# Kernel tuning notes

Hardware: AMD Instinct MI355X
Metric: run time of the kernel (lower is better)

Reference implementation:

```python
import jax, jax.numpy as jnp
import numpy as np

INPUT_DIM, CB_DIM, CB_VOCAB = 512, 16, 8192
N = 16384
EPS = 1e-12  # F.normalize default eps


def setup_inputs() -> dict:
    key = jax.random.key(0)
    kx, kp, kc = jax.random.split(key, 3)
    x = jax.random.normal(kx, (N, INPUT_DIM), dtype=jnp.float32)
    # xavier_uniform_ on P [input_dim, cb_dim]
    bound = float(np.sqrt(6.0 / (INPUT_DIM + CB_DIM)))
    P = jax.random.uniform(kp, (INPUT_DIM, CB_DIM), dtype=jnp.float32,
                           minval=-bound, maxval=bound)
    # CB = F.normalize(randn(cb_vocab, cb_dim)) -> unit rows
    CB = jax.random.normal(kc, (CB_VOCAB, CB_DIM), dtype=jnp.float32)
    CB = CB / jnp.maximum(jnp.linalg.norm(CB, axis=1, keepdims=True), EPS)
    return {"x": x, "P": P, "CB": CB}


def reference(x, P, CB):
    # random projection: [N, input_dim] @ [input_dim, cb_dim] -> [N, cb_dim]
    xp = x @ P
    # L2-normalize projected vectors (rows)
    xp = xp / jnp.maximum(jnp.linalg.norm(xp, axis=1, keepdims=True), EPS)
    # cosine similarity against unit-norm codebook = plain dot product
    sim = xp @ CB.T  # [N, cb_vocab]
    return jnp.argmax(sim, axis=1)  # [N] int codebook indices
```

## Files before the change

kernel.cpp:

```cpp
#include <hip/hip_runtime.h>
#include <stdint.h>

#define N_ROWS   16384
#define IN_DIM   512
#define CB_DIM   16
#define CB_VOCAB 8192

#define PREP_BLOCKS 128
#define PROJ_BLOCKS 256

#define N_RT   (N_ROWS / 16)
#define N_CT   (CB_VOCAB / 16)
#define CODEPARTS 32
#define CT_PER_PART (N_CT / CODEPARTS)
#define N_ROWGRP 64

#define WS_OFF_AFA  0
#define WS_OFF_AFB  (1u << 20)
#define WS_OFF_BHH  (2u << 20)
#define WS_OFF_B31  ((2u << 20) + (512u << 10))
#define WS_OFF_PART (3u << 20)
#define WS_OFF_CNT  ((3u << 20) + (128u << 10))
#define WS_OFF_PF   ((3u << 20) + (192u << 10))

typedef __attribute__((ext_vector_type(8))) short bf16x8;
typedef __attribute__((ext_vector_type(4))) float f32x4;

__device__ __forceinline__ unsigned fkey(float f) {
    unsigned u = __float_as_uint(f);
    return (u & 0x80000000u) ? ~u : (u | 0x80000000u);
}

__device__ __forceinline__ unsigned short f2bf(float f) {
    unsigned u = __float_as_uint(f);
    return (unsigned short)((u + 0x7FFFu + ((u >> 16) & 1u)) >> 16);
}
__device__ __forceinline__ float bf2f(unsigned short h) {
    return __uint_as_float(((unsigned)h) << 16);
}

__global__ __launch_bounds__(256, 2)
void k_prep(const float* __restrict__ P, const float* __restrict__ CB,
            bf16x8* __restrict__ Bhh, bf16x8* __restrict__ B31,
            bf16x8* __restrict__ Pf,
            unsigned long long* __restrict__ part, unsigned* __restrict__ cnt) {
    const int pb   = blockIdx.x;
    const int wave = threadIdx.x >> 6;
    const int lane = threadIdx.x & 63;

    if (threadIdx.x < 128) part[pb * 128 + threadIdx.x] = 0ull;
    if (pb == 0 && threadIdx.x < 64) cnt[threadIdx.x] = 0u;

    {
        const int ct   = pb * 4 + wave;
        const int n    = lane & 15;
        const int quad = lane >> 4;
        const int kh   = (quad & 1) * 8;
        const int lvl  = quad >> 1;
        const int code = ct * 16 + n;

        const float4* b4 = (const float4*)(CB + (size_t)code * CB_DIM + kh);
        float4 a = b4[0], b = b4[1];
        float v[8] = {a.x, a.y, a.z, a.w, b.x, b.y, b.z, b.w};

        bf16x8 shh, s31;
#pragma unroll
        for (int j = 0; j < 8; ++j) {
            float f = v[j];
            unsigned short b1 = f2bf(f);  float r1 = f - bf2f(b1);
            unsigned short b2 = f2bf(r1); float r2 = r1 - bf2f(b2);
            unsigned short b3 = f2bf(r2);
            shh[j] = (short)(lvl ? b2 : b1);
            s31[j] = (short)(lvl ? b1 : b3);
        }
        Bhh[(size_t)ct * 64 + lane] = shh;
        B31[(size_t)ct * 64 + lane] = s31;
    }

    const int gslot = pb * 256 + threadIdx.x;
    if (gslot < 1024) {
        const int c  = gslot >> 6;
        const int l  = gslot & 63;
        const int n  = l & 15;
        const int kq = l >> 4;
        const int k0 = c * 32 + kq * 8;

        bf16x8 p1, p2, p3;
#pragma unroll
        for (int j = 0; j < 8; ++j) {
            float f = P[(size_t)(k0 + j) * CB_DIM + n];
            unsigned short b1 = f2bf(f);  float r1 = f - bf2f(b1);
            unsigned short b2 = f2bf(r1); float r2 = r1 - bf2f(b2);
            unsigned short b3 = f2bf(r2);
            p1[j] = (short)b1; p2[j] = (short)b2; p3[j] = (short)b3;
        }
        Pf[gslot]        = p1;
        Pf[1024 + gslot] = p2;
        Pf[2048 + gslot] = p3;
    }
}

__global__ __launch_bounds__(256, 1)
void k_proj(const float* __restrict__ x, const bf16x8* __restrict__ Pf,
            bf16x8* __restrict__ AfragA, bf16x8* __restrict__ AfragB) {
    __shared__ float xpL[4][16][20];
    const int wave = threadIdx.x >> 6;
    const int lane = threadIdx.x & 63;
    const int rt   = blockIdx.x * 4 + wave;
    const int m    = lane & 15;
    const int kq   = lane >> 4;

    const float4* xr =
        (const float4*)(x + (size_t)(rt * 16 + m) * IN_DIM) + kq * 2;

    f32x4 acc1 = {0.f, 0.f, 0.f, 0.f};
    f32x4 acc2 = {0.f, 0.f, 0.f, 0.f};

    float4 xf0[4], xf1[4];
#pragma unroll
    for (int c = 0; c < 4; ++c) { xf0[c] = xr[c * 8]; xf1[c] = xr[c * 8 + 1]; }

#pragma unroll
    for (int c = 0; c < 16; ++c) {
        bf16x8 p1 = Pf[c * 64 + lane];
        bf16x8 p2 = Pf[1024 + c * 64 + lane];
        bf16x8 p3 = Pf[2048 + c * 64 + lane];

        float4 xa = xf0[c & 3], xb = xf1[c & 3];
        if (c + 4 < 16) {
            xf0[c & 3] = xr[(c + 4) * 8];
            xf1[c & 3] = xr[(c + 4) * 8 + 1];
        }

        float xs[8] = {xa.x, xa.y, xa.z, xa.w, xb.x, xb.y, xb.z, xb.w};
        bf16x8 a1, a2, a3;
#pragma unroll
        for (int j = 0; j < 8; ++j) {
            float f = xs[j];
            unsigned short b1 = f2bf(f);  float r1 = f - bf2f(b1);
            unsigned short b2 = f2bf(r1); float r2 = r1 - bf2f(b2);
            unsigned short b3 = f2bf(r2);
            a1[j] = (short)b1; a2[j] = (short)b2; a3[j] = (short)b3;
        }

        acc1 = __builtin_amdgcn_mfma_f32_16x16x32_bf16(a1, p1, acc1, 0, 0, 0);
        acc2 = __builtin_amdgcn_mfma_f32_16x16x32_bf16(a1, p2, acc2, 0, 0, 0);
        acc1 = __builtin_amdgcn_mfma_f32_16x16x32_bf16(a2, p1, acc1, 0, 0, 0);
        acc2 = __builtin_amdgcn_mfma_f32_16x16x32_bf16(a1, p3, acc2, 0, 0, 0);
        acc1 = __builtin_amdgcn_mfma_f32_16x16x32_bf16(a2, p2, acc1, 0, 0, 0);
        acc2 = __builtin_amdgcn_mfma_f32_16x16x32_bf16(a3, p1, acc2, 0, 0, 0);
    }

#pragma unroll
    for (int r = 0; r < 4; ++r)
        xpL[wave][kq * 4 + r][m] = acc1[r] + acc2[r];

    asm volatile("s_waitcnt lgkmcnt(0)" ::: "memory");
    __builtin_amdgcn_sched_barrier(0);

    const int kh  = (kq & 1) * 8;
    const int lvl = kq >> 1;
    bf16x8 sa, sb;
#pragma unroll
    for (int j = 0; j < 8; ++j) {
        float f = xpL[wave][m][kh + j];
        unsigned short b1 = f2bf(f);  float r1 = f - bf2f(b1);
        unsigned short b2 = f2bf(r1); float r2 = r1 - bf2f(b2);
        unsigned short b3 = f2bf(r2);
        sa[j] = (short)(lvl ? b2 : b1);
        sb[j] = (short)(lvl ? b3 : b1);
    }
    AfragA[(size_t)rt * 64 + lane] = sa;
    AfragB[(size_t)rt * 64 + lane] = sb;
}

__global__ __launch_bounds__(256, 4)
void k_scan(const bf16x8* __restrict__ AfragA, const bf16x8* __restrict__ AfragB,
            const bf16x8* __restrict__ Bhh, const bf16x8* __restrict__ B31,
            unsigned long long* __restrict__ part, unsigned* __restrict__ cnt,
            int* __restrict__ out) {
    __shared__ int s_done;
    const int codepart = blockIdx.x & (CODEPARTS - 1);
    const int rowgrp   = blockIdx.x >> 5;
    const int wave     = threadIdx.x >> 6;
    const int lane     = threadIdx.x & 63;
    const int n        = lane & 15;
    const int quad     = lane >> 4;
    const int rt_base  = rowgrp * 16 + wave * 4;

    bf16x8 Aa[4], Ab[4];
#pragma unroll
    for (int t = 0; t < 4; ++t) {
        Aa[t] = AfragA[(size_t)(rt_base + t) * 64 + lane];
        Ab[t] = AfragB[(size_t)(rt_base + t) * 64 + lane];
    }

    float bestv[4][4];
    int   bestc[4][4];
#pragma unroll
    for (int t = 0; t < 4; ++t)
#pragma unroll
        for (int r = 0; r < 4; ++r) { bestv[t][r] = -INFINITY; bestc[t][r] = 0; }

    const int ct0 = codepart * CT_PER_PART;
    size_t ib = (size_t)ct0 * 64;
    bf16x8 nb1  = Bhh[ib + lane];
    bf16x8 nb1s = Bhh[ib + (lane ^ 32)];
    bf16x8 nb3  = B31[ib + lane];

    for (int c = 0; c < CT_PER_PART; ++c) {
        bf16x8 b1 = nb1, b1s = nb1s, b3 = nb3;
        if (c + 1 < CT_PER_PART) {
            size_t ibn = (size_t)(ct0 + c + 1) * 64;
            nb1  = Bhh[ibn + lane];
            nb1s = Bhh[ibn + (lane ^ 32)];
            nb3  = B31[ibn + lane];
        }
#pragma unroll
        for (int t = 0; t < 4; ++t) {
            f32x4 s = __builtin_amdgcn_mfma_f32_16x16x32_bf16(
                          Aa[t], b1, (f32x4){0.f, 0.f, 0.f, 0.f}, 0, 0, 0);
            s = __builtin_amdgcn_mfma_f32_16x16x32_bf16(Aa[t], b1s, s, 0, 0, 0);
            s = __builtin_amdgcn_mfma_f32_16x16x32_bf16(Ab[t], b3,  s, 0, 0, 0);
#pragma unroll
            for (int r = 0; r < 4; ++r) {
                if (s[r] > bestv[t][r]) { bestv[t][r] = s[r]; bestc[t][r] = c; }
            }
        }
    }

#pragma unroll
    for (int t = 0; t < 4; ++t) {
#pragma unroll
        for (int r = 0; r < 4; ++r) {
            unsigned code = (unsigned)(codepart * (CT_PER_PART * 16) +
                                       bestc[t][r] * 16 + n);
            unsigned long long packed =
                ((unsigned long long)fkey(bestv[t][r]) << 32) |
                (unsigned long long)(0xFFFFFFFFu - code);
#pragma unroll
            for (int mk = 1; mk <= 8; mk <<= 1) {
                unsigned long long o = __shfl_xor(packed, mk, 64);
                packed = (o > packed) ? o : packed;
            }
            if (n == 0) {
                int row = (rt_base + t) * 16 + quad * 4 + r;
                atomicMax(&part[row], packed);
            }
        }
    }

    __syncthreads();
    if (threadIdx.x == 0)
        s_done = (atomicAdd(&cnt[rowgrp], 1u) == (unsigned)(CODEPARTS - 1));
    __syncthreads();

    if (s_done) {
        int row = rowgrp * 256 + threadIdx.x;
        unsigned long long v = atomicAdd(&part[row], 0ull);
        out[row] = (int)(0xFFFFFFFFu - (unsigned)(v & 0xFFFFFFFFull));
    }
}

extern "C" void kernel_launch(void* const* d_in, const int* in_sizes, int n_in,
                              void* d_out, int out_size, void* d_ws, size_t ws_size,
                              hipStream_t stream) {
    const float* x  = (const float*)d_in[0];
    const float* P  = (const float*)d_in[1];
    const float* CB = (const float*)d_in[2];
    int* out = (int*)d_out;

    char* ws = (char*)d_ws;
    bf16x8* AfragA = (bf16x8*)(ws + WS_OFF_AFA);
    bf16x8* AfragB = (bf16x8*)(ws + WS_OFF_AFB);
    bf16x8* Bhh    = (bf16x8*)(ws + WS_OFF_BHH);
    bf16x8* B31    = (bf16x8*)(ws + WS_OFF_B31);
    unsigned long long* part = (unsigned long long*)(ws + WS_OFF_PART);
    unsigned* cnt  = (unsigned*)(ws + WS_OFF_CNT);
    bf16x8* Pf     = (bf16x8*)(ws + WS_OFF_PF);

    k_prep<<<PREP_BLOCKS, 256, 0, stream>>>(P, CB, Bhh, B31, Pf, part, cnt);
    k_proj<<<PROJ_BLOCKS, 256, 0, stream>>>(x, Pf, AfragA, AfragB);
    k_scan<<<N_ROWGRP * CODEPARTS, 256, 0, stream>>>(
        AfragA, AfragB, Bhh, B31, part, cnt, out);
}
```

Before: 121.1 us.

## Fuse prep and projection kernels, split K across waves, deepen scan prefetch

Merges the codebook/P preprocessing kernel and the projection kernel into one launch. Each projection block now rebuilds the split-bf16 P fragments in shared memory and splits the K dimension across four waves, then reduces them through LDS. Codebook-conversion blocks run alongside as extra blocks. The scan kernel's codebook prefetch becomes two tiles deep and the loop is fully unrolled. This removes one launch and the inter-kernel dependency, and raises parallelism in the projection. In exchange, every one of the 1024 projection blocks redundantly converts P, and register pressure in the scan loop goes up.

```diff
diff --git a/kernel.cpp b/kernel.cpp
--- a/kernel.cpp
+++ b/kernel.cpp
@@ -6,10 +6,9 @@
 #define CB_DIM   16
 #define CB_VOCAB 8192
 
+#define PROJ_BLOCKS 1024
 #define PREP_BLOCKS 128
-#define PROJ_BLOCKS 256
-
-#define N_RT   (N_ROWS / 16)
+
 #define N_CT   (CB_VOCAB / 16)
 #define CODEPARTS 32
 #define CT_PER_PART (N_CT / CODEPARTS)
@@ -21,7 +20,6 @@
 #define WS_OFF_B31  ((2u << 20) + (512u << 10))
 #define WS_OFF_PART (3u << 20)
 #define WS_OFF_CNT  ((3u << 20) + (128u << 10))
-#define WS_OFF_PF   ((3u << 20) + (192u << 10))
 
 typedef __attribute__((ext_vector_type(8))) short bf16x8;
 typedef __attribute__((ext_vector_type(4))) float f32x4;
@@ -39,19 +37,24 @@
     return __uint_as_float(((unsigned)h) << 16);
 }
 
-__global__ __launch_bounds__(256, 2)
-void k_prep(const float* __restrict__ P, const float* __restrict__ CB,
-            bf16x8* __restrict__ Bhh, bf16x8* __restrict__ B31,
-            bf16x8* __restrict__ Pf,
-            unsigned long long* __restrict__ part, unsigned* __restrict__ cnt) {
-    const int pb   = blockIdx.x;
-    const int wave = threadIdx.x >> 6;
-    const int lane = threadIdx.x & 63;
-
-    if (threadIdx.x < 128) part[pb * 128 + threadIdx.x] = 0ull;
-    if (pb == 0 && threadIdx.x < 64) cnt[threadIdx.x] = 0u;
-
-    {
+__global__ __launch_bounds__(256, 3)
+void k_front(const float* __restrict__ x, const float* __restrict__ P,
+             const float* __restrict__ CB,
+             bf16x8* __restrict__ AfragA, bf16x8* __restrict__ AfragB,
+             bf16x8* __restrict__ Bhh, bf16x8* __restrict__ B31,
+             unsigned long long* __restrict__ part, unsigned* __restrict__ cnt) {
+    __shared__ bf16x8 sPf[3][1024];
+    __shared__ __align__(16) float foldb[1024];
+
+    const int tid  = threadIdx.x;
+    const int wave = tid >> 6;
+    const int lane = tid & 63;
+
+    if (blockIdx.x >= PROJ_BLOCKS) {
+        const int pb = blockIdx.x - PROJ_BLOCKS;
+        if (tid < 128) part[pb * 128 + tid] = 0ull;
+        if (pb == 0 && tid < 64) cnt[tid] = 0u;
+
         const int ct   = pb * 4 + wave;
         const int n    = lane & 15;
         const int quad = lane >> 4;
@@ -75,12 +78,14 @@
         }
         Bhh[(size_t)ct * 64 + lane] = shh;
         B31[(size_t)ct * 64 + lane] = s31;
-    }
-
-    const int gslot = pb * 256 + threadIdx.x;
-    if (gslot < 1024) {
-        const int c  = gslot >> 6;
-        const int l  = gslot & 63;
+        return;
+    }
+
+#pragma unroll
+    for (int s4 = 0; s4 < 4; ++s4) {
+        const int s  = tid + s4 * 256;
+        const int c  = s >> 6;
+        const int l  = s & 63;
         const int n  = l & 15;
         const int kq = l >> 4;
         const int k0 = c * 32 + kq * 8;
@@ -94,44 +99,33 @@
             unsigned short b3 = f2bf(r2);
             p1[j] = (short)b1; p2[j] = (short)b2; p3[j] = (short)b3;
         }
-        Pf[gslot]        = p1;
-        Pf[1024 + gslot] = p2;
-        Pf[2048 + gslot] = p3;
-    }
-}
-
-__global__ __launch_bounds__(256, 1)
-void k_proj(const float* __restrict__ x, const bf16x8* __restrict__ Pf,
-            bf16x8* __restrict__ AfragA, bf16x8* __restrict__ AfragB) {
-    __shared__ float xpL[4][16][20];
-    const int wave = threadIdx.x >> 6;
-    const int lane = threadIdx.x & 63;
-    const int rt   = blockIdx.x * 4 + wave;
-    const int m    = lane & 15;
-    const int kq   = lane >> 4;
-
-    const float4* xr =
-        (const float4*)(x + (size_t)(rt * 16 + m) * IN_DIM) + kq * 2;
+        sPf[0][s] = p1; sPf[1][s] = p2; sPf[2][s] = p3;
+    }
+    __syncthreads();
+
+    const int rt = blockIdx.x;
+    const int m  = lane & 15;
+    const int kq = lane >> 4;
+    const float4* xr = (const float4*)(x + (size_t)(rt * 16 + m) * IN_DIM);
+
+    float4 xf[8];
+#pragma unroll
+    for (int i = 0; i < 4; ++i) {
+        xf[2 * i]     = xr[(wave * 4 + i) * 8 + kq * 2];
+        xf[2 * i + 1] = xr[(wave * 4 + i) * 8 + kq * 2 + 1];
+    }
 
     f32x4 acc1 = {0.f, 0.f, 0.f, 0.f};
     f32x4 acc2 = {0.f, 0.f, 0.f, 0.f};
 
-    float4 xf0[4], xf1[4];
-#pragma unroll
-    for (int c = 0; c < 4; ++c) { xf0[c] = xr[c * 8]; xf1[c] = xr[c * 8 + 1]; }
-
-#pragma unroll
-    for (int c = 0; c < 16; ++c) {
-        bf16x8 p1 = Pf[c * 64 + lane];
-        bf16x8 p2 = Pf[1024 + c * 64 + lane];
-        bf16x8 p3 = Pf[2048 + c * 64 + lane];
-
-        float4 xa = xf0[c & 3], xb = xf1[c & 3];
-        if (c + 4 < 16) {
-            xf0[c & 3] = xr[(c + 4) * 8];
-            xf1[c & 3] = xr[(c + 4) * 8 + 1];
-        }
-
+#pragma unroll
+    for (int i = 0; i < 4; ++i) {
+        const int c = wave * 4 + i;
+        bf16x8 p1 = sPf[0][c * 64 + lane];
+        bf16x8 p2 = sPf[1][c * 64 + lane];
+        bf16x8 p3 = sPf[2][c * 64 + lane];
+
+        float4 xa = xf[2 * i], xb = xf[2 * i + 1];
         float xs[8] = {xa.x, xa.y, xa.z, xa.w, xb.x, xb.y, xb.z, xb.w};
         bf16x8 a1, a2, a3;
 #pragma unroll
@@ -151,27 +145,41 @@
         acc2 = __builtin_amdgcn_mfma_f32_16x16x32_bf16(a3, p1, acc2, 0, 0, 0);
     }
 
-#pragma unroll
-    for (int r = 0; r < 4; ++r)
-        xpL[wave][kq * 4 + r][m] = acc1[r] + acc2[r];
-
-    asm volatile("s_waitcnt lgkmcnt(0)" ::: "memory");
-    __builtin_amdgcn_sched_barrier(0);
-
-    const int kh  = (kq & 1) * 8;
-    const int lvl = kq >> 1;
-    bf16x8 sa, sb;
-#pragma unroll
-    for (int j = 0; j < 8; ++j) {
-        float f = xpL[wave][m][kh + j];
-        unsigned short b1 = f2bf(f);  float r1 = f - bf2f(b1);
-        unsigned short b2 = f2bf(r1); float r2 = r1 - bf2f(b2);
-        unsigned short b3 = f2bf(r2);
-        sa[j] = (short)(lvl ? b2 : b1);
-        sb[j] = (short)(lvl ? b3 : b1);
-    }
-    AfragA[(size_t)rt * 64 + lane] = sa;
-    AfragB[(size_t)rt * 64 + lane] = sb;
+    *(f32x4*)&foldb[(wave * 64 + lane) * 4] = acc1 + acc2;
+    __syncthreads();
+
+    if (wave == 0) {
+        f32x4 s0 = *(const f32x4*)&foldb[(0 * 64 + lane) * 4];
+        f32x4 s1 = *(const f32x4*)&foldb[(1 * 64 + lane) * 4];
+        f32x4 s2 = *(const f32x4*)&foldb[(2 * 64 + lane) * 4];
+        f32x4 s3 = *(const f32x4*)&foldb[(3 * 64 + lane) * 4];
+        f32x4 sum = ((s0 + s1) + s2) + s3;
+
+        asm volatile("s_waitcnt lgkmcnt(0)" ::: "memory");
+        __builtin_amdgcn_sched_barrier(0);
+
+#pragma unroll
+        for (int r = 0; r < 4; ++r)
+            foldb[(kq * 4 + r) * 20 + m] = sum[r];
+
+        asm volatile("s_waitcnt lgkmcnt(0)" ::: "memory");
+        __builtin_amdgcn_sched_barrier(0);
+
+        const int kh  = (kq & 1) * 8;
+        const int lvl = kq >> 1;
+        bf16x8 sa, sb;
+#pragma unroll
+        for (int j = 0; j < 8; ++j) {
+            float f = foldb[m * 20 + kh + j];
+            unsigned short b1 = f2bf(f);  float r1 = f - bf2f(b1);
+            unsigned short b2 = f2bf(r1); float r2 = r1 - bf2f(b2);
+            unsigned short b3 = f2bf(r2);
+            sa[j] = (short)(lvl ? b2 : b1);
+            sb[j] = (short)(lvl ? b3 : b1);
+        }
+        AfragA[(size_t)rt * 64 + lane] = sa;
+        AfragB[(size_t)rt * 64 + lane] = sb;
+    }
 }
 
 __global__ __launch_bounds__(256, 4)
@@ -203,23 +211,28 @@
         for (int r = 0; r < 4; ++r) { bestv[t][r] = -INFINITY; bestc[t][r] = 0; }
 
     const int ct0 = codepart * CT_PER_PART;
-    size_t ib = (size_t)ct0 * 64;
-    bf16x8 nb1  = Bhh[ib + lane];
-    bf16x8 nb1s = Bhh[ib + (lane ^ 32)];
-    bf16x8 nb3  = B31[ib + lane];
-
+    const bf16x8* pB1  = Bhh + (size_t)ct0 * 64 + lane;
+    const bf16x8* pB1s = Bhh + (size_t)ct0 * 64 + (lane ^ 32);
+    const bf16x8* pB3  = B31 + (size_t)ct0 * 64 + lane;
+
+    const f32x4 zero = {0.f, 0.f, 0.f, 0.f};
+
+    bf16x8 rb1[2], rb1s[2], rb3[2];
+    rb1[0]  = pB1[0];   rb1[1]  = pB1[64];
+    rb1s[0] = pB1s[0];  rb1s[1] = pB1s[64];
+    rb3[0]  = pB3[0];   rb3[1]  = pB3[64];
+
+#pragma unroll
     for (int c = 0; c < CT_PER_PART; ++c) {
-        bf16x8 b1 = nb1, b1s = nb1s, b3 = nb3;
-        if (c + 1 < CT_PER_PART) {
-            size_t ibn = (size_t)(ct0 + c + 1) * 64;
-            nb1  = Bhh[ibn + lane];
-            nb1s = Bhh[ibn + (lane ^ 32)];
-            nb3  = B31[ibn + lane];
+        bf16x8 b1 = rb1[c & 1], b1s = rb1s[c & 1], b3 = rb3[c & 1];
+        if (c + 2 < CT_PER_PART) {
+            rb1[c & 1]  = pB1[(c + 2) * 64];
+            rb1s[c & 1] = pB1s[(c + 2) * 64];
+            rb3[c & 1]  = pB3[(c + 2) * 64];
         }
 #pragma unroll
         for (int t = 0; t < 4; ++t) {
-            f32x4 s = __builtin_amdgcn_mfma_f32_16x16x32_bf16(
-                          Aa[t], b1, (f32x4){0.f, 0.f, 0.f, 0.f}, 0, 0, 0);
+            f32x4 s = __builtin_amdgcn_mfma_f32_16x16x32_bf16(Aa[t], b1, zero, 0, 0, 0);
             s = __builtin_amdgcn_mfma_f32_16x16x32_bf16(Aa[t], b1s, s, 0, 0, 0);
             s = __builtin_amdgcn_mfma_f32_16x16x32_bf16(Ab[t], b3,  s, 0, 0, 0);
 #pragma unroll
@@ -277,10 +290,9 @@
     bf16x8* B31    = (bf16x8*)(ws + WS_OFF_B31);
     unsigned long long* part = (unsigned long long*)(ws + WS_OFF_PART);
     unsigned* cnt  = (unsigned*)(ws + WS_OFF_CNT);
-    bf16x8* Pf     = (bf16x8*)(ws + WS_OFF_PF);
-
-    k_prep<<<PREP_BLOCKS, 256, 0, stream>>>(P, CB, Bhh, B31, Pf, part, cnt);
-    k_proj<<<PROJ_BLOCKS, 256, 0, stream>>>(x, Pf, AfragA, AfragB);
+
+    k_front<<<PROJ_BLOCKS + PREP_BLOCKS, 256, 0, stream>>>(
+        x, P, CB, AfragA, AfragB, Bhh, B31, part, cnt);
     k_scan<<<N_ROWGRP * CODEPARTS, 256, 0, stream>>>(
         AfragA, AfragB, Bhh, B31, part, cnt, out);
 }
```

After: 262.9 us. 2.17x slower.
